# Kernel tuning notes

Hardware: AMD Instinct MI355X
Metric: run time of the kernel (lower is better)

The kernel has to match this reference:

```python
import jax, jax.numpy as jnp
import numpy as np

DIM = 512
HEADS = 8
HEAD_DIM = DIM // HEADS
LN_EPS = 1e-5


def setup_inputs() -> dict:
    key = jax.random.key(0)
    ks = jax.random.split(key, 16)
    B, L, E = 4, 4096, DIM
    x = jax.random.normal(ks[0], (B, L, E), dtype=jnp.float32)
    w = lambda k: jax.random.normal(k, (E, E), dtype=jnp.float32) * 0.02
    b = lambda k: jax.random.normal(k, (E,), dtype=jnp.float32) * 0.02
    return {
        "x": x,
        "ln_gamma": jnp.ones((E,), jnp.float32),
        "ln_beta": jnp.zeros((E,), jnp.float32),
        "Wqr": w(ks[1]), "bqr": b(ks[2]),
        "Wqi": w(ks[3]), "bqi": b(ks[4]),
        "Wkr": w(ks[5]), "bkr": b(ks[6]),
        "Wki": w(ks[7]), "bki": b(ks[8]),
        "Wvr": w(ks[9]), "bvr": b(ks[10]),
        "Wvi": w(ks[11]), "bvi": b(ks[12]),
        "Wo": w(ks[13]),
    }


def reference(x, ln_gamma, ln_beta, Wqr, bqr, Wqi, bqi, Wkr, bkr, Wki, bki,
              Wvr, bvr, Wvi, bvi, Wo):
    B, L, E = x.shape
    H, d = HEADS, HEAD_DIM
    # LayerNorm over last dim
    mu = jnp.mean(x, axis=-1, keepdims=True)
    var = jnp.mean(jnp.square(x - mu), axis=-1, keepdims=True)
    xn = (x - mu) * jax.lax.rsqrt(var + LN_EPS) * ln_gamma + ln_beta
    # rfft along time dim -> F = L//2 + 1 frequency bins
    xf = jnp.fft.rfft(xn, axis=1, norm="ortho")
    xr, xi = jnp.real(xf), jnp.imag(xf)  # [B, F, E]
    # split real/imag QKV projections (torch Linear: y = x @ W.T + b)
    Qr = xr @ Wqr.T + bqr
    Qi = xi @ Wqi.T + bqi
    Kr = xr @ Wkr.T + bkr
    Ki = xi @ Wki.T + bki
    Vr = xr @ Wvr.T + bvr
    Vi = xi @ Wvi.T + bvi
    Fn = xr.shape[1]
    split = lambda t: t.reshape(B, Fn, H, d)  # b l (h d) -> b l h d
    Qr, Qi, Kr, Ki, Vr, Vi = map(split, (Qr, Qi, Kr, Ki, Vr, Vi))
    # scores = Qr.Kr + Qi.Ki, scaled softmax over keys
    scores = (jnp.einsum("blhd,bmhd->bhlm", Qr, Kr)
              + jnp.einsum("blhd,bmhd->bhlm", Qi, Ki))
    attn = jax.nn.softmax(scores * (d ** -0.5), axis=-1)
    out_r = jnp.einsum("bhlm,bmhd->bhld", attn, Vr)
    out_i = jnp.einsum("bhlm,bmhd->bhld", attn, Vi)
    out_f = jax.lax.complex(out_r, out_i)  # [B, H, F, d]
    out_f = jnp.transpose(out_f, (0, 2, 1, 3)).reshape(B, Fn, E)
    out_t = jnp.fft.irfft(out_f, n=L, axis=1, norm="ortho")
    return out_t @ Wo.T
```

## Files before the change

kernel.cpp:

```cpp
#include <hip/hip_runtime.h>
#include <math.h>

#define NB 4
#define NL 4096
#define NE 512
#define NH 8
#define ND 64
#define NF 2049
#define WSZ (NE * NE)
#define QPAD 2176
#define OPSZ ((long)NB * NH * QPAD * 64)

static constexpr float INV_SQRT_N = 1.0f / 64.0f;

typedef __attribute__((ext_vector_type(8))) short bf16x8;
typedef __attribute__((ext_vector_type(4))) short short4v;
typedef __attribute__((ext_vector_type(4))) float f32x4;

__device__ __forceinline__ float2 cmul(float2 a, float2 b) {
    return make_float2(a.x * b.x - a.y * b.y, a.x * b.y + a.y * b.x);
}

__device__ __forceinline__ short cvt_bf16(float f) {
    unsigned u = __float_as_uint(f);
    unsigned r = (u + 0x7FFFu + ((u >> 16) & 1u)) >> 16;
    return (short)r;
}

__device__ __forceinline__ int pack_bf16x2(float a, float b) {
    return (int)(unsigned short)cvt_bf16(a) | ((int)(unsigned short)cvt_bf16(b) << 16);
}

__device__ __forceinline__ short4v pk4(float a, float b, float c, float d) {
    union { unsigned u[2]; short4v s; } r;
    asm("v_cvt_pk_bf16_f32 %0, %1, %2" : "=v"(r.u[0]) : "v"(a), "v"(b));
    asm("v_cvt_pk_bf16_f32 %0, %1, %2" : "=v"(r.u[1]) : "v"(c), "v"(d));
    return r.s;
}

__device__ __forceinline__ float2 unpk(int v) {
    return make_float2(__uint_as_float(((unsigned)v & 0xffffu) << 16),
                       __uint_as_float((unsigned)v & 0xffff0000u));
}

__device__ __forceinline__ int b4rev(int t) {
    int r = __brev((unsigned)t) >> 20;
    return ((r & 0x555) << 1) | ((r & 0xAAA) >> 1);
}

__global__ __launch_bounds__(256) void twiddle_kernel(float2* __restrict__ twg) {
    int j = blockIdx.x * 256 + threadIdx.x;
    double ang = (2.0 * M_PI / (double)NL) * (double)j;
    double s, c;
    sincos(ang, &s, &c);
    twg[j] = make_float2((float)c, (float)s);
}

__global__ __launch_bounds__(256) void castw_kernel(
    const float* __restrict__ w0, const float* __restrict__ w1,
    const float* __restrict__ w2, const float* __restrict__ w3,
    const float* __restrict__ w4, const float* __restrict__ w5,
    const float* __restrict__ w6, short* __restrict__ dst) {
    int which = blockIdx.y;
    const float* s = which == 0 ? w0 : which == 1 ? w1 : which == 2 ? w2 :
                     which == 3 ? w3 : which == 4 ? w4 : which == 5 ? w5 : w6;
    long i = (long)blockIdx.x * 1024 + threadIdx.x * 4;
    float4 v = *(const float4*)(s + i);
    short4v o = {cvt_bf16(v.x), cvt_bf16(v.y), cvt_bf16(v.z), cvt_bf16(v.w)};
    *(short4v*)(dst + (long)which * WSZ + i) = o;
}

__global__ __launch_bounds__(256) void ln_kernel(
    const float* __restrict__ x, const float* __restrict__ g,
    const float* __restrict__ be, short* __restrict__ xnb) {
    int wv = threadIdx.x >> 6, lane = threadIdx.x & 63;
    long row = (long)blockIdx.x * 4 + wv;
    const float* xp = x + row * NE + lane * 8;
    float4 a = *(const float4*)xp;
    float4 b = *(const float4*)(xp + 4);
    float s  = a.x + a.y + a.z + a.w + b.x + b.y + b.z + b.w;
    float ss = a.x * a.x + a.y * a.y + a.z * a.z + a.w * a.w
             + b.x * b.x + b.y * b.y + b.z * b.z + b.w * b.w;
#pragma unroll
    for (int o = 32; o; o >>= 1) { s += __shfl_xor(s, o); ss += __shfl_xor(ss, o); }
    float mu = s * (1.0f / NE);
    float var = ss * (1.0f / NE) - mu * mu;
    float rs = rsqrtf(var + 1e-5f);
    const float* gp = g + lane * 8;
    const float* bp = be + lane * 8;
    float4 g0 = *(const float4*)gp, g1 = *(const float4*)(gp + 4);
    float4 b0 = *(const float4*)bp, b1 = *(const float4*)(bp + 4);
    bf16x8 ov;
    ov[0] = cvt_bf16((a.x - mu) * rs * g0.x + b0.x);
    ov[1] = cvt_bf16((a.y - mu) * rs * g0.y + b0.y);
    ov[2] = cvt_bf16((a.z - mu) * rs * g0.z + b0.z);
    ov[3] = cvt_bf16((a.w - mu) * rs * g0.w + b0.w);
    ov[4] = cvt_bf16((b.x - mu) * rs * g1.x + b1.x);
    ov[5] = cvt_bf16((b.y - mu) * rs * g1.y + b1.y);
    ov[6] = cvt_bf16((b.z - mu) * rs * g1.z + b1.z);
    ov[7] = cvt_bf16((b.w - mu) * rs * g1.w + b1.w);
    *(bf16x8*)(xnb + row * NE + lane * 8) = ov;
}

template <int INV>
__device__ __forceinline__ void fft4_stages(float2* sdata, const float2* tws, int tid) {
#pragma unroll
    for (int st = 0; st < 6; ++st) {
        __syncthreads();
        int Q = 1 << (2 * st);
        int tq = 10 - 2 * st;
#pragma unroll
        for (int jj = 0; jj < 4; ++jj) {
            int j = tid + jj * 256;
            int k = j & (Q - 1);
            int i0 = ((j >> (2 * st)) << (2 * st + 2)) | k;
            float2 w1 = tws[k << tq];
            float2 w2 = tws[(2 * k) << tq];
            float2 w3 = cmul(w1, w2);
            float2 a = sdata[i0];
            float2 b = cmul(w1, sdata[i0 + Q]);
            float2 c = cmul(w2, sdata[i0 + 2 * Q]);
            float2 d = cmul(w3, sdata[i0 + 3 * Q]);
            float2 t0 = make_float2(a.x + c.x, a.y + c.y);
            float2 t1 = make_float2(a.x - c.x, a.y - c.y);
            float2 t2 = make_float2(b.x + d.x, b.y + d.y);
            float2 bd = make_float2(b.x - d.x, b.y - d.y);
            float2 t3 = INV ? make_float2(-bd.y, bd.x) : make_float2(bd.y, -bd.x);
            sdata[i0]         = make_float2(t0.x + t2.x, t0.y + t2.y);
            sdata[i0 + Q]     = make_float2(t1.x + t3.x, t1.y + t3.y);
            sdata[i0 + 2 * Q] = make_float2(t0.x - t2.x, t0.y - t2.y);
            sdata[i0 + 3 * Q] = make_float2(t1.x - t3.x, t1.y - t3.y);
        }
    }
    __syncthreads();
}

__device__ __forceinline__ int ep_swizzle(int loc) {
    return ((loc & 7) << 5) | (loc >> 3);
}

__global__ __launch_bounds__(256) void rfft_pair(
    const short* __restrict__ xnb, const float2* __restrict__ twg,
    short* __restrict__ xr, short* __restrict__ xi) {
    __shared__ float2 sdata[NL];
    __shared__ float2 tws[NL / 2];
    int b = blockIdx.x >> 8;
    int e0 = ep_swizzle(blockIdx.x & 255) * 2;
    int tid = threadIdx.x;
    const short* xp = xnb + (long)b * NL * NE + e0;
#pragma unroll
    for (int jj = 0; jj < 16; ++jj) {
        int t = tid + jj * 256;
        int v = *(const int*)(xp + (long)t * NE);
        sdata[b4rev(t)] = unpk(v);
    }
#pragma unroll
    for (int jj = 0; jj < 8; ++jj) {
        int j = tid + jj * 256;
        float2 w = twg[j];
        tws[j] = make_float2(w.x, -w.y);
    }
    fft4_stages<0>(sdata, tws, tid);
    short* xrp = xr + (long)b * NF * NE + e0;
    short* xip = xi + (long)b * NF * NE + e0;
    for (int f = tid; f < NF; f += 256) {
        int M = (NL - f) & (NL - 1);
        float2 zf = sdata[f], zm = sdata[M];
        float re0 = (zf.x + zm.x) * (0.5f * INV_SQRT_N);
        float im0 = (zf.y - zm.y) * (0.5f * INV_SQRT_N);
        float re1 = (zf.y + zm.y) * (0.5f * INV_SQRT_N);
        float im1 = (zm.x - zf.x) * (0.5f * INV_SQRT_N);
        *(int*)(xrp + (long)f * NE) = pack_bf16x2(re0, re1);
        *(int*)(xip + (long)f * NE) = pack_bf16x2(im0, im1);
    }
}

__global__ __launch_bounds__(256) void irfft_pair(
    const float* __restrict__ Opr, const float* __restrict__ Opi,
    const float* __restrict__ lsp, const float2* __restrict__ twg,
    short* __restrict__ yt) {
    __shared__ float2 sdata[NL];
    __shared__ float2 tws[NL / 2];
    int b = blockIdx.x >> 8;
    int e0 = ep_swizzle(blockIdx.x & 255) * 2;
    int tid = threadIdx.x;
    int h = e0 >> 6, d0 = e0 & 63;
    long p0 = ((long)b * NH + h) * ((long)QPAD * 64) + d0;
    long p1 = ((long)(NB + b) * NH + h) * ((long)QPAD * 64) + d0;
    long l0 = ((long)b * NH + h) * QPAD;
    long l1 = ((long)(NB + b) * NH + h) * QPAD;
    for (int f = tid; f < NF; f += 256) {
        float l = lsp[l0 + f] + lsp[l1 + f];
        float inv = 1.0f / l;
        float2 r1 = *(const float2*)(Opr + p0 + (long)f * 64);
        float2 r2 = *(const float2*)(Opr + p1 + (long)f * 64);
        float2 i1 = *(const float2*)(Opi + p0 + (long)f * 64);
        float2 i2 = *(const float2*)(Opi + p1 + (long)f * 64);
        float2 vr = make_float2((r1.x + r2.x) * inv, (r1.y + r2.y) * inv);
        float2 vi = make_float2((i1.x + i2.x) * inv, (i1.y + i2.y) * inv);
        if (f == 0 || f == NL / 2) vi = make_float2(0.f, 0.f);
        sdata[b4rev(f)] = make_float2(vr.x - vi.y, vi.x + vr.y);
        if (f > 0 && f < NL / 2) {
            sdata[b4rev(NL - f)] = make_float2(vr.x + vi.y, vr.y - vi.x);
        }
    }
#pragma unroll
    for (int jj = 0; jj < 8; ++jj) {
        int j = tid + jj * 256;
        tws[j] = twg[j];
    }
    fft4_stages<1>(sdata, tws, tid);
    short* yp = yt + (long)b * NL * NE + e0;
#pragma unroll
    for (int jj = 0; jj < 16; ++jj) {
        int t = tid + jj * 256;
        float2 z = sdata[t];
        *(int*)(yp + (long)t * NE) = pack_bf16x2(z.x * INV_SQRT_N, z.y * INV_SQRT_N);
    }
}

__device__ __forceinline__ void gemm_core(
    const short* __restrict__ A, const short* __restrict__ W,
    const float* __restrict__ bias, float scale, short* __restrict__ Cb,
    float* __restrict__ Cf, int N) {
    __shared__ short As[128][40];
    __shared__ short Bs[128][40];
    int o0 = blockIdx.x * 128;
    int n0 = blockIdx.y * 128;
    int tid = threadIdx.x;
    int lane = tid & 63, wv = tid >> 6;
    int quad = lane >> 4, cl = lane & 15;
    int rbase = (wv >> 1) << 6;
    int cbase = (wv & 1) << 6;
    int srow = tid >> 2;
    int sseg = tid & 3;
    f32x4 acc[4][4];
#pragma unroll
    for (int i = 0; i < 4; ++i)
#pragma unroll
        for (int j = 0; j < 4; ++j) acc[i][j] = (f32x4){0, 0, 0, 0};

    int ra = n0 + srow;      if (ra >= N) ra = N - 1;
    int rb = n0 + srow + 64; if (rb >= N) rb = N - 1;
    const short* Ap0 = A + (long)ra * NE + sseg * 8;
    const short* Ap1 = A + (long)rb * NE + sseg * 8;
    const short* Wp0 = W + (long)(o0 + srow) * NE + sseg * 8;
    const short* Wp1 = W + (long)(o0 + srow + 64) * NE + sseg * 8;

    bf16x8 a0 = *(const bf16x8*)Ap0, a1 = *(const bf16x8*)Ap1;
    bf16x8 b0 = *(const bf16x8*)Wp0, b1 = *(const bf16x8*)Wp1;

    for (int kt = 0; kt < 16; ++kt) {
        __syncthreads();
        *(bf16x8*)&As[srow][sseg * 8] = a0;
        *(bf16x8*)&As[srow + 64][sseg * 8] = a1;
        *(bf16x8*)&Bs[srow][sseg * 8] = b0;
        *(bf16x8*)&Bs[srow + 64][sseg * 8] = b1;
        __syncthreads();
        if (kt < 15) {
            int ko = (kt + 1) * 32;
            a0 = *(const bf16x8*)(Ap0 + ko);
            a1 = *(const bf16x8*)(Ap1 + ko);
            b0 = *(const bf16x8*)(Wp0 + ko);
            b1 = *(const bf16x8*)(Wp1 + ko);
        }
        bf16x8 ar[4], br[4];
#pragma unroll
        for (int i = 0; i < 4; ++i) ar[i] = *(const bf16x8*)&As[rbase + 16 * i + cl][quad * 8];
#pragma unroll
        for (int j = 0; j < 4; ++j) br[j] = *(const bf16x8*)&Bs[cbase + 16 * j + cl][quad * 8];
#pragma unroll
        for (int i = 0; i < 4; ++i)
#pragma unroll
            for (int j = 0; j < 4; ++j)
                acc[i][j] = __builtin_amdgcn_mfma_f32_16x16x32_bf16(ar[i], br[j], acc[i][j], 0, 0, 0);
    }
    float bv[4];
#pragma unroll
    for (int j = 0; j < 4; ++j) bv[j] = bias ? bias[o0 + cbase + 16 * j + cl] : 0.0f;
#pragma unroll
    for (int i = 0; i < 4; ++i) {
#pragma unroll
        for (int r = 0; r < 4; ++r) {
            int n = n0 + rbase + 16 * i + quad * 4 + r;
            if (n >= N) continue;
#pragma unroll
            for (int j = 0; j < 4; ++j) {
                float v = (acc[i][j][r] + bv[j]) * scale;
                int o = o0 + cbase + 16 * j + cl;
                if (Cb) Cb[(long)n * NE + o] = cvt_bf16(v);
                else    Cf[(long)n * NE + o] = v;
            }
        }
    }
}

__global__ __launch_bounds__(256) void gemm_qkv(
    const short* __restrict__ A,
    const short* __restrict__ W0, const short* __restrict__ W1, const short* __restrict__ W2,
    const float* __restrict__ b0, const float* __restrict__ b1, const float* __restrict__ b2,
    short* __restrict__ C0, short* __restrict__ C1, short* __restrict__ C2, int N) {
    int z = blockIdx.z;
    const short* W = z == 0 ? W0 : z == 1 ? W1 : W2;
    const float* bb = z == 0 ? b0 : z == 1 ? b1 : b2;
    short* C = z == 0 ? C0 : z == 1 ? C1 : C2;
    gemm_core(A, W, bb, z == 0 ? 0.125f : 1.0f, C, nullptr, N);
}

__global__ __launch_bounds__(256) void gemm_out(
    const short* __restrict__ A, const short* __restrict__ W,
    float* __restrict__ C, int N) {
    gemm_core(A, W, nullptr, 1.0f, nullptr, C, N);
}

__global__ __launch_bounds__(256) void fattn_mfma(
    const short* __restrict__ Qr, const short* __restrict__ Qi,
    const short* __restrict__ Kr, const short* __restrict__ Ki,
    const short* __restrict__ Vr, const short* __restrict__ Vi,
    float* __restrict__ Opr, float* __restrict__ Opi, float* __restrict__ lsp) {
    __shared__ short Ks[2][64][72];
    __shared__ short Vt[2][64][72];
    int tid = threadIdx.x;
    int wv = tid >> 6, lane = tid & 63;
    int quad = lane >> 4, cl = lane & 15;
    int h = blockIdx.y;
    int zz = blockIdx.z;
    int b = zz >> 1, half = zz & 1;
    long base = (long)b * NF * NE + h * ND;
    int qbase = blockIdx.x * 128 + wv * 32;
    int kt0 = half * 17;
    int ktN = half ? 33 : 17;

    int sk0 = (tid >> 4) << 2;
    int sd0 = (tid & 15) << 2;
    int g0 = tid >> 4;
    int dsw = tid & 15;

    bf16x8 qar[2][2], qai[2][2];
#pragma unroll
    for (int u = 0; u < 2; ++u) {
        int qrow = qbase + 16 * u + cl; if (qrow >= NF) qrow = NF - 1;
        const short* pr = Qr + base + (long)qrow * NE + 8 * quad;
        const short* pi = Qi + base + (long)qrow * NE + 8 * quad;
        qar[u][0] = *(const bf16x8*)pr;
        qar[u][1] = *(const bf16x8*)(pr + 32);
        qai[u][0] = *(const bf16x8*)pi;
        qai[u][1] = *(const bf16x8*)(pi + 32);
    }

    float ls[2] = {0.f, 0.f};
    f32x4 Or2[4][2], Oi2[4][2];
#pragma unroll
    for (int t = 0; t < 4; ++t)
#pragma unroll
        for (int u = 0; u < 2; ++u) {
            Or2[t][u] = (f32x4){0, 0, 0, 0};
            Oi2[t][u] = (f32x4){0, 0, 0, 0};
        }

    short4v lk0[4], lk1[4], lv0[4], lv1[4];
    const long TSTEP = (long)64 * NE;
    const short* pKr = Kr + base + (long)sk0 * NE + sd0 + (long)kt0 * TSTEP;
    const short* pKi = Ki + base + (long)sk0 * NE + sd0 + (long)kt0 * TSTEP;
    const short* pVr = Vr + base + (long)sk0 * NE + sd0 + (long)kt0 * TSTEP;
    const short* pVi = Vi + base + (long)sk0 * NE + sd0 + (long)kt0 * TSTEP;

    auto ldfull = [&]() {
#pragma unroll
        for (int kk = 0; kk < 4; ++kk) {
            long o = (long)kk * NE;
            lk0[kk] = *(const short4v*)(pKr + o);
            lk1[kk] = *(const short4v*)(pKi + o);
            lv0[kk] = *(const short4v*)(pVr + o);
            lv1[kk] = *(const short4v*)(pVi + o);
        }
        pKr += TSTEP; pKi += TSTEP; pVr += TSTEP; pVi += TSTEP;
    };
    auto ldmask = [&]() {
        short4v z4 = {0, 0, 0, 0};
#pragma unroll
        for (int kk = 0; kk < 4; ++kk) {
            int mg = 2048 + sk0 + kk;
            if (mg < NF) {
                long o = (long)kk * NE;
                lk0[kk] = *(const short4v*)(pKr + o);
                lk1[kk] = *(const short4v*)(pKi + o);
                lv0[kk] = *(const short4v*)(pVr + o);
                lv1[kk] = *(const short4v*)(pVi + o);
            } else { lk0[kk] = z4; lk1[kk] = z4; lv0[kk] = z4; lv1[kk] = z4; }
        }
    };
    ldfull();

    for (int kt = kt0; kt < ktN; ++kt) {
        __syncthreads();
#pragma unroll
        for (int kk = 0; kk < 4; ++kk) {
            *(short4v*)&Ks[0][sk0 + kk][sd0] = lk0[kk];
            *(short4v*)&Ks[1][sk0 + kk][sd0] = lk1[kk];
        }
        {
            int cv = (g0 ^ dsw) << 2;
#pragma unroll
            for (int dd = 0; dd < 4; ++dd) {
                short4v t0 = {lv0[0][dd], lv0[1][dd], lv0[2][dd], lv0[3][dd]};
                *(short4v*)&Vt[0][sd0 + dd][cv] = t0;
                short4v t1 = {lv1[0][dd], lv1[1][dd], lv1[2][dd], lv1[3][dd]};
                *(short4v*)&Vt[1][sd0 + dd][cv] = t1;
            }
        }
        __syncthreads();
        if (kt + 1 < ktN) {
            if (kt + 1 < 32) ldfull();
            else ldmask();
        }

        f32x4 c[4][2];
        __builtin_amdgcn_s_setprio(1);
#pragma unroll
        for (int t = 0; t < 4; ++t) {
            const short* kr = &Ks[0][cl + 16 * t][8 * quad];
            const short* ki = &Ks[1][cl + 16 * t][8 * quad];
            bf16x8 k0 = *(const bf16x8*)kr;
            bf16x8 k1 = *(const bf16x8*)(kr + 32);
            bf16x8 k2 = *(const bf16x8*)ki;
            bf16x8 k3 = *(const bf16x8*)(ki + 32);
#pragma unroll
            for (int u = 0; u < 2; ++u) {
                f32x4 acc = (f32x4){0, 0, 0, 0};
                acc = __builtin_amdgcn_mfma_f32_16x16x32_bf16(k0, qar[u][0], acc, 0, 0, 0);
                acc = __builtin_amdgcn_mfma_f32_16x16x32_bf16(k1, qar[u][1], acc, 0, 0, 0);
                acc = __builtin_amdgcn_mfma_f32_16x16x32_bf16(k2, qai[u][0], acc, 0, 0, 0);
                acc = __builtin_amdgcn_mfma_f32_16x16x32_bf16(k3, qai[u][1], acc, 0, 0, 0);
                c[t][u] = acc;
            }
        }
        __builtin_amdgcn_s_setprio(0);

        short4v pb[4][2];
        if (kt < 32) {
#pragma unroll
            for (int t = 0; t < 4; ++t)
#pragma unroll
                for (int u = 0; u < 2; ++u) {
                    float p0 = __expf(c[t][u][0]);
                    float p1 = __expf(c[t][u][1]);
                    float p2 = __expf(c[t][u][2]);
                    float p3 = __expf(c[t][u][3]);
                    ls[u] += (p0 + p1) + (p2 + p3);
                    pb[t][u] = pk4(p0, p1, p2, p3);
                }
        } else {
#pragma unroll
            for (int t = 0; t < 4; ++t) {
                int kbase = 2048 + 16 * t + quad * 4;
#pragma unroll
                for (int u = 0; u < 2; ++u) {
                    float p0 = (kbase + 0 < NF) ? __expf(c[t][u][0]) : 0.0f;
                    float p1 = (kbase + 1 < NF) ? __expf(c[t][u][1]) : 0.0f;
                    float p2 = (kbase + 2 < NF) ? __expf(c[t][u][2]) : 0.0f;
                    float p3 = (kbase + 3 < NF) ? __expf(c[t][u][3]) : 0.0f;
                    ls[u] += (p0 + p1) + (p2 + p3);
                    pb[t][u] = pk4(p0, p1, p2, p3);
                }
            }
        }

        __builtin_amdgcn_s_setprio(1);
#pragma unroll
        for (int nt = 0; nt < 4; ++nt) {
            int d = cl + 16 * nt;
            int dg = (d >> 2) & 15;
#pragma unroll
            for (int t = 0; t < 4; ++t) {
                int g = 4 * t + quad;
                int cv = ((g ^ dg) << 2);
                short4v va = *(const short4v*)&Vt[0][d][cv];
                short4v vb = *(const short4v*)&Vt[1][d][cv];
#pragma unroll
                for (int u = 0; u < 2; ++u) {
                    Or2[nt][u] = __builtin_amdgcn_mfma_f32_16x16x16bf16_1k(va, pb[t][u], Or2[nt][u], 0, 0, 0);
                    Oi2[nt][u] = __builtin_amdgcn_mfma_f32_16x16x16bf16_1k(vb, pb[t][u], Oi2[nt][u], 0, 0, 0);
                }
            }
        }
        __builtin_amdgcn_s_setprio(0);
    }

    long ob = ((long)(half * NB + b) * NH + h) * ((long)QPAD * 64);
    long lb = ((long)(half * NB + b) * NH + h) * QPAD;
#pragma unroll
    for (int u = 0; u < 2; ++u) {
        float l2 = ls[u];
        l2 += __shfl_xor(l2, 16);
        l2 += __shfl_xor(l2, 32);
        int q = qbase + 16 * u + cl;
        if (q < NF) {
            if (quad == 0) lsp[lb + q] = l2;
            float* pr = Opr + ob + (long)q * 64;
            float* pi2 = Opi + ob + (long)q * 64;
#pragma unroll
            for (int nt = 0; nt < 4; ++nt) {
                int d0 = 16 * nt + quad * 4;
                *(f32x4*)(pr + d0) = Or2[nt][u];
                *(f32x4*)(pi2 + d0) = Oi2[nt][u];
            }
        }
    }
}

extern "C" void kernel_launch(void* const* d_in, const int* in_sizes, int n_in,
                              void* d_out, int out_size, void* d_ws, size_t ws_size,
                              hipStream_t stream) {
    const float* x   = (const float*)d_in[0];
    const float* g   = (const float*)d_in[1];
    const float* be  = (const float*)d_in[2];
    const float* Wqr = (const float*)d_in[3];
    const float* bqr = (const float*)d_in[4];
    const float* Wqi = (const float*)d_in[5];
    const float* bqi = (const float*)d_in[6];
    const float* Wkr = (const float*)d_in[7];
    const float* bkr = (const float*)d_in[8];
    const float* Wki = (const float*)d_in[9];
    const float* bki = (const float*)d_in[10];
    const float* Wvr = (const float*)d_in[11];
    const float* bvr = (const float*)d_in[12];
    const float* Wvi = (const float*)d_in[13];
    const float* bvi = (const float*)d_in[14];
    const float* Wo  = (const float*)d_in[15];
    float* out = (float*)d_out;

    const long SZ_T = (long)NB * NL * NE;
    const long SZ_F = (long)NB * NF * NE;
    float2* twg = (float2*)d_ws;
    short* xnb = (short*)(twg + 2048);
    short* xr  = xnb + SZ_T;
    short* xi  = xr + SZ_F;
    short* Qr  = xi + SZ_F;
    short* Qi  = Qr + SZ_F;
    short* Kr  = Qi + SZ_F;
    short* Ki  = Kr + SZ_F;
    short* Vr  = Ki + SZ_F;
    short* Vi  = Vr + SZ_F;
    short* Orb = Vi + SZ_F;
    short* Oib = Orb + SZ_F;
    short* yt  = Oib + SZ_F;
    short* wb  = yt + SZ_T;
    float* Opr = (float*)(wb + 7L * WSZ);
    float* Opi = Opr + 2 * OPSZ;
    float* lsp = Opi + 2 * OPSZ;
    (void)Orb; (void)Oib;

    twiddle_kernel<<<NL / 2 / 256, 256, 0, stream>>>(twg);
    castw_kernel<<<dim3(WSZ / 1024, 7), 256, 0, stream>>>(Wqr, Wqi, Wkr, Wki, Wvr, Wvi, Wo, wb);
    ln_kernel<<<NB * NL / 4, 256, 0, stream>>>(x, g, be, xnb);
    rfft_pair<<<NB * 256, 256, 0, stream>>>(xnb, twg, xr, xi);
    int Nf = NB * NF;
    dim3 gq(NE / 128, (Nf + 127) / 128, 3);
    gemm_qkv<<<gq, 256, 0, stream>>>(xr, wb + 0L * WSZ, wb + 2L * WSZ, wb + 4L * WSZ,
                                     bqr, bkr, bvr, Qr, Kr, Vr, Nf);
    gemm_qkv<<<gq, 256, 0, stream>>>(xi, wb + 1L * WSZ, wb + 3L * WSZ, wb + 5L * WSZ,
                                     bqi, bki, bvi, Qi, Ki, Vi, Nf);
    fattn_mfma<<<dim3(17, NH, NB * 2), 256, 0, stream>>>(Qr, Qi, Kr, Ki, Vr, Vi, Opr, Opi, lsp);
    irfft_pair<<<NB * 256, 256, 0, stream>>>(Opr, Opi, lsp, twg, yt);
    gemm_out<<<dim3(NE / 128, NB * NL / 128), 256, 0, stream>>>(yt, wb + 6L * WSZ, out, NB * NL);
}
```

Measured before the change: 429.7 us.

## Use direct global-to-LDS loads in GEMM core and merge QKV launches

The GEMM core now stages A and W tiles with global_load_lds (16 bytes per lane) straight into unpadded shared memory, replacing the register-staged prefetch and LDS stores. The two QKV projection launches are merged into one launch with six z-slices that pick real or imaginary inputs, weights and biases. This is meant to cut VGPR traffic and LDS store instructions and to remove one kernel launch. In exchange, the register prefetch that overlapped the next tile's loads with MFMA work is gone, and removing the row padding may add LDS bank conflicts on the fragment reads.

```diff
diff --git a/kernel.cpp b/kernel.cpp
--- a/kernel.cpp
+++ b/kernel.cpp
@@ -36,6 +36,12 @@
     asm("v_cvt_pk_bf16_f32 %0, %1, %2" : "=v"(r.u[0]) : "v"(a), "v"(b));
     asm("v_cvt_pk_bf16_f32 %0, %1, %2" : "=v"(r.u[1]) : "v"(c), "v"(d));
     return r.s;
+}
+
+__device__ __forceinline__ void load_lds16(const void* g, void* l) {
+    __builtin_amdgcn_global_load_lds(
+        (const __attribute__((address_space(1))) void*)g,
+        (__attribute__((address_space(3))) void*)l, 16, 0, 0);
 }
 
 __device__ __forceinline__ float2 unpk(int v) {
@@ -223,8 +229,8 @@
     const short* __restrict__ A, const short* __restrict__ W,
     const float* __restrict__ bias, float scale, short* __restrict__ Cb,
     float* __restrict__ Cf, int N) {
-    __shared__ short As[128][40];
-    __shared__ short Bs[128][40];
+    __shared__ short As[128][32];
+    __shared__ short Bs[128][32];
     int o0 = blockIdx.x * 128;
     int n0 = blockIdx.y * 128;
     int tid = threadIdx.x;
@@ -232,38 +238,34 @@
     int quad = lane >> 4, cl = lane & 15;
     int rbase = (wv >> 1) << 6;
     int cbase = (wv & 1) << 6;
-    int srow = tid >> 2;
-    int sseg = tid & 3;
+
+    int srow = wv * 32 + (lane >> 2);
+    int scol = (lane & 3) * 8;
+    int ra0 = n0 + srow;      if (ra0 >= N) ra0 = N - 1;
+    int ra1 = n0 + srow + 16; if (ra1 >= N) ra1 = N - 1;
+    const short* Asrc0 = A + (long)ra0 * NE + scol;
+    const short* Asrc1 = A + (long)ra1 * NE + scol;
+    const short* Wsrc0 = W + (long)(o0 + srow) * NE + scol;
+    const short* Wsrc1 = W + (long)(o0 + srow + 16) * NE + scol;
+    short* Adst0 = &As[wv * 32][0];
+    short* Adst1 = &As[wv * 32 + 16][0];
+    short* Bdst0 = &Bs[wv * 32][0];
+    short* Bdst1 = &Bs[wv * 32 + 16][0];
+
     f32x4 acc[4][4];
 #pragma unroll
     for (int i = 0; i < 4; ++i)
 #pragma unroll
         for (int j = 0; j < 4; ++j) acc[i][j] = (f32x4){0, 0, 0, 0};
-
-    int ra = n0 + srow;      if (ra >= N) ra = N - 1;
-    int rb = n0 + srow + 64; if (rb >= N) rb = N - 1;
-    const short* Ap0 = A + (long)ra * NE + sseg * 8;
-    const short* Ap1 = A + (long)rb * NE + sseg * 8;
-    const short* Wp0 = W + (long)(o0 + srow) * NE + sseg * 8;
-    const short* Wp1 = W + (long)(o0 + srow + 64) * NE + sseg * 8;
-
-    bf16x8 a0 = *(const bf16x8*)Ap0, a1 = *(const bf16x8*)Ap1;
-    bf16x8 b0 = *(const bf16x8*)Wp0, b1 = *(const bf16x8*)Wp1;
 
     for (int kt = 0; kt < 16; ++kt) {
         __syncthreads();
-        *(bf16x8*)&As[srow][sseg * 8] = a0;
-        *(bf16x8*)&As[srow + 64][sseg * 8] = a1;
-        *(bf16x8*)&Bs[srow][sseg * 8] = b0;
-        *(bf16x8*)&Bs[srow + 64][sseg * 8] = b1;
+        load_lds16(Asrc0, Adst0);
+        load_lds16(Asrc1, Adst1);
+        load_lds16(Wsrc0, Bdst0);
+        load_lds16(Wsrc1, Bdst1);
+        Asrc0 += 32; Asrc1 += 32; Wsrc0 += 32; Wsrc1 += 32;
         __syncthreads();
-        if (kt < 15) {
-            int ko = (kt + 1) * 32;
-            a0 = *(const bf16x8*)(Ap0 + ko);
-            a1 = *(const bf16x8*)(Ap1 + ko);
-            b0 = *(const bf16x8*)(Wp0 + ko);
-            b1 = *(const bf16x8*)(Wp1 + ko);
-        }
         bf16x8 ar[4], br[4];
 #pragma unroll
         for (int i = 0; i < 4; ++i) ar[i] = *(const bf16x8*)&As[rbase + 16 * i + cl][quad * 8];
@@ -296,15 +298,25 @@
 }
 
 __global__ __launch_bounds__(256) void gemm_qkv(
-    const short* __restrict__ A,
-    const short* __restrict__ W0, const short* __restrict__ W1, const short* __restrict__ W2,
-    const float* __restrict__ b0, const float* __restrict__ b1, const float* __restrict__ b2,
-    short* __restrict__ C0, short* __restrict__ C1, short* __restrict__ C2, int N) {
+    const short* __restrict__ Ar, const short* __restrict__ Ai,
+    const short* __restrict__ wb,
+    const float* __restrict__ bqr, const float* __restrict__ bqi,
+    const float* __restrict__ bkr, const float* __restrict__ bki,
+    const float* __restrict__ bvr, const float* __restrict__ bvi,
+    short* __restrict__ Qr, short* __restrict__ Qi,
+    short* __restrict__ Kr, short* __restrict__ Ki,
+    short* __restrict__ Vr, short* __restrict__ Vi, int N) {
     int z = blockIdx.z;
-    const short* W = z == 0 ? W0 : z == 1 ? W1 : W2;
-    const float* bb = z == 0 ? b0 : z == 1 ? b1 : b2;
-    short* C = z == 0 ? C0 : z == 1 ? C1 : C2;
-    gemm_core(A, W, bb, z == 0 ? 0.125f : 1.0f, C, nullptr, N);
+    int comp = z % 3, im = z / 3;
+    const short* A = im ? Ai : Ar;
+    const short* W = wb + (long)(comp * 2 + im) * WSZ;
+    const float* bb = comp == 0 ? (im ? bqi : bqr)
+                    : comp == 1 ? (im ? bki : bkr)
+                                : (im ? bvi : bvr);
+    short* C = comp == 0 ? (im ? Qi : Qr)
+             : comp == 1 ? (im ? Ki : Kr)
+                         : (im ? Vi : Vr);
+    gemm_core(A, W, bb, comp == 0 ? 0.125f : 1.0f, C, nullptr, N);
 }
 
 __global__ __launch_bounds__(256) void gemm_out(
@@ -556,11 +568,9 @@
     ln_kernel<<<NB * NL / 4, 256, 0, stream>>>(x, g, be, xnb);
     rfft_pair<<<NB * 256, 256, 0, stream>>>(xnb, twg, xr, xi);
     int Nf = NB * NF;
-    dim3 gq(NE / 128, (Nf + 127) / 128, 3);
-    gemm_qkv<<<gq, 256, 0, stream>>>(xr, wb + 0L * WSZ, wb + 2L * WSZ, wb + 4L * WSZ,
-                                     bqr, bkr, bvr, Qr, Kr, Vr, Nf);
-    gemm_qkv<<<gq, 256, 0, stream>>>(xi, wb + 1L * WSZ, wb + 3L * WSZ, wb + 5L * WSZ,
-                                     bqi, bki, bvi, Qi, Ki, Vi, Nf);
+    dim3 gq(NE / 128, (Nf + 127) / 128, 6);
+    gemm_qkv<<<gq, 256, 0, stream>>>(xr, xi, wb, bqr, bqi, bkr, bki, bvr, bvi,
+                                     Qr, Qi, Kr, Ki, Vr, Vi, Nf);
     fattn_mfma<<<dim3(17, NH, NB * 2), 256, 0, stream>>>(Qr, Qi, Kr, Ki, Vr, Vi, Opr, Opi, lsp);
     irfft_pair<<<NB * 256, 256, 0, stream>>>(Opr, Opi, lsp, twg, yt);
     gemm_out<<<dim3(NE / 128, NB * NL / 128), 256, 0, stream>>>(yt, wb + 6L * WSZ, out, NB * NL);
```

New measurement: 410.8 us. -4.4%, faster.
